# Performance work log

Measured on AMD Instinct MI355X. Metric: run time of the kernel, lower is better.

Reference implementation:

```python
import jax, jax.numpy as jnp
import numpy as np

D_MODEL = 1024
N_STATE = 64
BASEWIDTH = 3
BC_SCALE = (D_MODEL / BASEWIDTH) ** -0.5  # 'mup' mode width_mult**-0.5
RMS_EPS = 1.1920928955078125e-07  # torch.finfo(float32).eps (RMSNorm eps=None default)


def setup_inputs() -> dict:
    key = jax.random.key(0)
    k1, k2, k3, k4 = jax.random.split(key, 4)
    Bsz, L = 4, 2048
    u = jax.random.normal(k1, (Bsz, D_MODEL, L), dtype=jnp.float32)
    A = jax.random.uniform(k2, (N_STATE,), dtype=jnp.float32) * 0.1  # buffer: rand(N)*A_scale
    B = (jax.random.normal(k3, (N_STATE, D_MODEL), dtype=jnp.float32) + 0.1) * BC_SCALE
    C = (jax.random.normal(k4, (N_STATE, D_MODEL), dtype=jnp.float32) + 0.1) * BC_SCALE
    D = jnp.ones((D_MODEL,), dtype=jnp.float32)
    norm_w = jnp.ones((D_MODEL,), dtype=jnp.float32)
    return {"L": L, "u": u, "A": A, "B": B, "C": C, "D": D, "norm_w": norm_w}


def _ssm(u, A, B, C, D, norm_w):
    # u: [b, d, l]
    scale = BC_SCALE  # applied to Bu, Cu in 'mup' hyperparam mode
    Bu = jnp.einsum('nd,bdl->bnl', B, u) * scale  # [b, n, l]
    Cu = jnp.einsum('nd,bdl->bnl', C, u) * scale  # [b, n, l]
    b, d, l = u.shape
    # shifted_delta == 1 (delta path commented out in source), so
    # h_{t} = A * h_{t-1} + Bu[:, :, t] (outer) u[:, :, t]
    h0 = jnp.zeros((b, d, A.shape[0]), dtype=u.dtype)

    def step(h, xs):
        bu_t, cu_t, u_t = xs  # [b,n], [b,n], [b,d]
        h = h * A + u_t[:, :, None] * bu_t[:, None, :]  # [b, d, n]
        y_t = jnp.einsum('bn,bdn->bd', cu_t, h)
        return h, y_t

    xs = (jnp.moveaxis(Bu, 2, 0), jnp.moveaxis(Cu, 2, 0), jnp.moveaxis(u, 2, 0))
    _, y = jax.lax.scan(step, h0, xs)  # y: [l, b, d]
    y = jnp.moveaxis(y, 0, 2).transpose(1, 0, 2) if False else jnp.transpose(y, (1, 2, 0))  # [b, d, l]
    out = y + u * D[None, :, None]
    # RMSNorm over d_model (apply in [b, l, d] layout)
    x = jnp.transpose(out, (0, 2, 1))  # [b, l, d]
    ms = jnp.mean(x * x, axis=-1, keepdims=True)
    x = x * jax.lax.rsqrt(ms + RMS_EPS) * norm_w
    return jnp.transpose(x, (0, 2, 1))  # [b, d, l]


def reference(L, u, A, B, C, D, norm_w):
    del L  # sequence length == u.shape[-1]
    return _ssm(u, A, B, C, D, norm_w)
```

## Files before the change

kernel.cpp:

```cpp
#include <hip/hip_runtime.h>
#include <stdint.h>

#define DM 1024
#define LS 2048
#define RMS_EPS 1.1920928955078125e-07f
#define S2 0.0029296875f

typedef __attribute__((ext_vector_type(8))) short bf16x8;
typedef __attribute__((ext_vector_type(4))) float f32x4;

__device__ __forceinline__ unsigned short f2bf(float f) {
  uint32_t u = __builtin_bit_cast(uint32_t, f);
  u += 0x7FFFu + ((u >> 16) & 1u);
  return (unsigned short)(u >> 16);
}

__global__ __launch_bounds__(256) void k0_prep(const float* __restrict__ B,
                                               const float* __restrict__ C,
                                               unsigned short* __restrict__ Bbf) {
  int i4 = blockIdx.x * 256 + threadIdx.x;
  const float4* src = (i4 < 16384) ? (const float4*)B : (const float4*)C;
  float4 v = src[i4 & 16383];
  ushort4 o;
  o.x = f2bf(v.x); o.y = f2bf(v.y); o.z = f2bf(v.z); o.w = f2bf(v.w);
  ((ushort4*)Bbf)[i4] = o;
}

__global__ __launch_bounds__(256) void kg(const float* __restrict__ u,
                                          const unsigned short* __restrict__ Bbf,
                                          const float* __restrict__ A,
                                          float* __restrict__ Kwg) {
  const int wg = blockIdx.x;
  const int sw = (wg & 7) * 64 + (wg >> 3);
  const int b  = sw >> 7;
  const int t0 = (sw & 127) * 16;
  const int tid  = threadIdx.x;
  const int lane = tid & 63;
  const int w    = tid >> 6;
  const int nn = lane & 15, q = lane >> 4;
  const float* ub = u + (size_t)b * DM * LS;

  __shared__ __align__(16) bf16x8 tile[128][32];
  __shared__ float KwS[16][20];
  float (*BuCu)[132] = (float (*)[132])&tile[0][0];

  {
    const int kq = lane >> 3;
    const int lo = lane & 7;
    const int gcol = t0 - 16 + 4*lo;
    #pragma unroll
    for (int hh = 0; hh < 4; ++hh) {
      const int krow = 256*w + 32*kq + 8*hh;
      float4 vv[8];
      if (gcol >= 0) {
        #pragma unroll
        for (int r = 0; r < 8; ++r)
          vv[r] = *(const float4*)(ub + (size_t)(krow + r) * LS + gcol);
      } else {
        #pragma unroll
        for (int r = 0; r < 8; ++r) vv[r] = make_float4(0.f, 0.f, 0.f, 0.f);
      }
      const int k8 = krow >> 3;
      #pragma unroll
      for (int c = 0; c < 4; ++c) {
        union { bf16x8 v; unsigned short s[8]; } t8;
        #pragma unroll
        for (int r = 0; r < 8; ++r) t8.s[r] = f2bf(((const float*)&vv[r])[c]);
        tile[k8][(4*lo + c) ^ kq] = t8.v;
      }
    }
  }
  __syncthreads();

  f32x4 acc[2][2] = {};
  const unsigned short* arow0 = Bbf + (size_t)(32*w + nn) * DM + 8*q;
  #pragma unroll 4
  for (int it = 0; it < 32; ++it) {
    const int sx = nn ^ (it & 7);
    bf16x8 bf1 = tile[4*it + q][16 + sx];
    bf16x8 af0 = *(const bf16x8*)(arow0 + 32*it);
    bf16x8 af1 = *(const bf16x8*)(arow0 + (size_t)16*DM + 32*it);
    acc[0][1] = __builtin_amdgcn_mfma_f32_16x16x32_bf16(af0, bf1, acc[0][1], 0, 0, 0);
    acc[1][1] = __builtin_amdgcn_mfma_f32_16x16x32_bf16(af1, bf1, acc[1][1], 0, 0, 0);
    if (w < 2) {
      bf16x8 bf0 = tile[4*it + q][sx];
      acc[0][0] = __builtin_amdgcn_mfma_f32_16x16x32_bf16(af0, bf0, acc[0][0], 0, 0, 0);
      acc[1][0] = __builtin_amdgcn_mfma_f32_16x16x32_bf16(af1, bf0, acc[1][0], 0, 0, 0);
    }
  }
  __syncthreads();

  #pragma unroll
  for (int rt = 0; rt < 2; ++rt)
    #pragma unroll
    for (int cn = 0; cn < 2; ++cn)
      *(f32x4*)&BuCu[16*cn + nn][32*w + 16*rt + 4*q] = acc[rt][cn];
  __syncthreads();

  {
    const int t = tid >> 4, p = tid & 15;
    const float4 cu = *(const float4*)&BuCu[16 + t][64 + 4*p];
    const float4 aa = *(const float4*)(A + 4*p);
    float pw0 = cu.x * S2, pw1 = cu.y * S2, pw2 = cu.z * S2, pw3 = cu.w * S2;
    #pragma unroll
    for (int j = 0; j < 16; ++j) {
      const float4 b4 = *(const float4*)&BuCu[16 + t - j][4*p];
      float s = pw0*b4.x + pw1*b4.y + pw2*b4.z + pw3*b4.w;
      s += __shfl_xor(s, 1, 64);
      s += __shfl_xor(s, 2, 64);
      s += __shfl_xor(s, 4, 64);
      s += __shfl_xor(s, 8, 64);
      if (p == 0) KwS[t][j] = s;
      pw0 *= aa.x; pw1 *= aa.y; pw2 *= aa.z; pw3 *= aa.w;
    }
  }
  __syncthreads();
  if (tid < 64) {
    const int t = tid >> 2, jq = tid & 3;
    *(float4*)(Kwg + ((size_t)b * LS + t0 + t) * 16 + 4*jq) =
        *(const float4*)&KwS[t][4*jq];
  }
}

__global__ __launch_bounds__(512) void kc(const float* __restrict__ u,
                                          const float* __restrict__ Kwg,
                                          const float* __restrict__ Dv,
                                          const float* __restrict__ nw,
                                          float* __restrict__ out) {
  const int wg = blockIdx.x;
  const int sw = (wg & 7) * 64 + (wg >> 3);
  const int b  = sw >> 7;
  const int t0 = (sw & 127) * 16;
  const int tid  = threadIdx.x;
  const int lane = tid & 63;
  const int w    = tid >> 6;
  const float* ub = u + (size_t)b * DM * LS;
  float* ob = out + (size_t)b * DM * LS;

  __shared__ float KwS[16][20];
  __shared__ float SSr[8][16];
  __shared__ float rsqv[16];

  if (tid < 64) {
    const int t = tid >> 2, jq = tid & 3;
    *(float4*)&KwS[t][4*jq] =
        *(const float4*)(Kwg + ((size_t)b * LS + t0 + t) * 16 + 4*jq);
  }
  __syncthreads();

  const int tg = tid & 3;
  const int dr = tid >> 2;
  const int cbase = t0 - 16 + 4*tg;
  float y[8][4];
  float ps[4] = {0.f, 0.f, 0.f, 0.f};
  #pragma unroll 1
  for (int c = 0; c < 8; ++c) {
    const int d = dr + 128*c;
    const float* rowp = ub + (size_t)d * LS;
    float wr[20];
    #pragma unroll
    for (int s5 = 0; s5 < 5; ++s5) {
      int g = cbase + 4*s5;
      float4 v = (g >= 0) ? *(const float4*)(rowp + g)
                          : make_float4(0.f, 0.f, 0.f, 0.f);
      wr[4*s5+0] = v.x; wr[4*s5+1] = v.y; wr[4*s5+2] = v.z; wr[4*s5+3] = v.w;
    }
    const float Dd = Dv[d];
    #pragma unroll
    for (int k = 0; k < 4; ++k) {
      f32x4 kv0 = *(const f32x4*)&KwS[4*tg + k][0];
      f32x4 kv1 = *(const f32x4*)&KwS[4*tg + k][4];
      f32x4 kv2 = *(const f32x4*)&KwS[4*tg + k][8];
      f32x4 kv3 = *(const f32x4*)&KwS[4*tg + k][12];
      float acc = wr[16 + k] * Dd;
      #pragma unroll
      for (int j = 0; j < 4; ++j)  acc = fmaf(kv0[j], wr[16 + k - j],      acc);
      #pragma unroll
      for (int j = 0; j < 4; ++j)  acc = fmaf(kv1[j], wr[16 + k - (j+4)],  acc);
      #pragma unroll
      for (int j = 0; j < 4; ++j)  acc = fmaf(kv2[j], wr[16 + k - (j+8)],  acc);
      #pragma unroll
      for (int j = 0; j < 4; ++j)  acc = fmaf(kv3[j], wr[16 + k - (j+12)], acc);
      y[c][k] = acc;
      ps[k] = fmaf(acc, acc, ps[k]);
    }
  }

  #pragma unroll
  for (int k = 0; k < 4; ++k) {
    ps[k] += __shfl_xor(ps[k], 4, 64);
    ps[k] += __shfl_xor(ps[k], 8, 64);
    ps[k] += __shfl_xor(ps[k], 16, 64);
    ps[k] += __shfl_xor(ps[k], 32, 64);
  }
  if (lane < 4)
    *(float4*)&SSr[w][4*lane] = make_float4(ps[0], ps[1], ps[2], ps[3]);
  __syncthreads();
  if (tid < 16) {
    float s = 0.f;
    #pragma unroll
    for (int ww = 0; ww < 8; ++ww) s += SSr[ww][tid];
    rsqv[tid] = rsqrtf(s * (1.f/1024.f) + RMS_EPS);
  }
  __syncthreads();

  float rq[4];
  #pragma unroll
  for (int k = 0; k < 4; ++k) rq[k] = rsqv[4*tg + k];
  #pragma unroll 1
  for (int c = 0; c < 8; ++c) {
    const int d = dr + 128*c;
    const float wn2 = nw[d];
    float4 o;
    o.x = y[c][0] * rq[0] * wn2;
    o.y = y[c][1] * rq[1] * wn2;
    o.z = y[c][2] * rq[2] * wn2;
    o.w = y[c][3] * rq[3] * wn2;
    *(float4*)(ob + (size_t)d * LS + t0 + 4*tg) = o;
  }
}

extern "C" void kernel_launch(void* const* d_in, const int* in_sizes, int n_in,
                              void* d_out, int out_size, void* d_ws, size_t ws_size,
                              hipStream_t stream) {
  const float* u  = (const float*)d_in[1];
  const float* A  = (const float*)d_in[2];
  const float* B  = (const float*)d_in[3];
  const float* C  = (const float*)d_in[4];
  const float* Dv = (const float*)d_in[5];
  const float* nw = (const float*)d_in[6];
  float* out = (float*)d_out;

  float* Kwg = (float*)d_ws;
  unsigned short* Bbf = (unsigned short*)((char*)d_ws + (512u << 10));

  k0_prep<<<dim3(128), dim3(256), 0, stream>>>(B, C, Bbf);
  kg     <<<dim3(512), dim3(256), 0, stream>>>(u, Bbf, A, Kwg);
  kc     <<<dim3(512), dim3(512), 0, stream>>>(u, Kwg, Dv, nw, out);
}
```

Baseline: 145.1 us.

## Fuse kernel-weight generation and causal convolution with RMSNorm into one kernel

Merges the kg and kc kernels so that each workgroup reuses the bf16 u tile already staged in LDS for the 16-tap causal convolution, D skip and RMSNorm. This removes the second full read of u from global memory, the Kwg workspace round trip and one kernel launch. Bu/Cu are now stored as bf16 in LDS, and the convolution reads bf16 u instead of fp32, which lowers precision of the output path. Work is remapped so each thread covers 4 channels by 16 timesteps, which raises register pressure.

```diff
diff --git a/kernel.cpp b/kernel.cpp
--- a/kernel.cpp
+++ b/kernel.cpp
@@ -13,6 +13,10 @@
   uint32_t u = __builtin_bit_cast(uint32_t, f);
   u += 0x7FFFu + ((u >> 16) & 1u);
   return (unsigned short)(u >> 16);
+}
+__device__ __forceinline__ float bf2f(unsigned short s) {
+  uint32_t u = ((uint32_t)s) << 16;
+  return __builtin_bit_cast(float, u);
 }
 
 __global__ __launch_bounds__(256) void k0_prep(const float* __restrict__ B,
@@ -26,10 +30,12 @@
   ((ushort4*)Bbf)[i4] = o;
 }
 
-__global__ __launch_bounds__(256) void kg(const float* __restrict__ u,
+__global__ __launch_bounds__(256) void kf(const float* __restrict__ u,
                                           const unsigned short* __restrict__ Bbf,
                                           const float* __restrict__ A,
-                                          float* __restrict__ Kwg) {
+                                          const float* __restrict__ Dv,
+                                          const float* __restrict__ nw,
+                                          float* __restrict__ out) {
   const int wg = blockIdx.x;
   const int sw = (wg & 7) * 64 + (wg >> 3);
   const int b  = sw >> 7;
@@ -41,8 +47,13 @@
   const float* ub = u + (size_t)b * DM * LS;
 
   __shared__ __align__(16) bf16x8 tile[128][32];
-  __shared__ float KwS[16][20];
-  float (*BuCu)[132] = (float (*)[132])&tile[0][0];
+  __shared__ __align__(16) unsigned short BuCuB[32][136];
+  __shared__ __align__(16) float Kwd[32][16];
+  __shared__ float SSr[4][16];
+  __shared__ float rsqv[16];
+
+  ((float*)Kwd)[tid]       = 0.f;
+  ((float*)Kwd)[tid + 256] = 0.f;
 
   {
     const int kq = lane >> 3;
@@ -74,7 +85,7 @@
 
   f32x4 acc[2][2] = {};
   const unsigned short* arow0 = Bbf + (size_t)(32*w + nn) * DM + 8*q;
-  #pragma unroll 4
+  #pragma unroll 8
   for (int it = 0; it < 32; ++it) {
     const int sx = nn ^ (it & 7);
     bf16x8 bf1 = tile[4*it + q][16 + sx];
@@ -88,135 +99,128 @@
       acc[1][0] = __builtin_amdgcn_mfma_f32_16x16x32_bf16(af1, bf0, acc[1][0], 0, 0, 0);
     }
   }
-  __syncthreads();
 
   #pragma unroll
   for (int rt = 0; rt < 2; ++rt)
     #pragma unroll
-    for (int cn = 0; cn < 2; ++cn)
-      *(f32x4*)&BuCu[16*cn + nn][32*w + 16*rt + 4*q] = acc[rt][cn];
+    for (int cn = 0; cn < 2; ++cn) {
+      ushort4 pk;
+      pk.x = f2bf(acc[rt][cn][0]); pk.y = f2bf(acc[rt][cn][1]);
+      pk.z = f2bf(acc[rt][cn][2]); pk.w = f2bf(acc[rt][cn][3]);
+      *(ushort4*)&BuCuB[16*cn + nn][32*w + 16*rt + 4*q] = pk;
+    }
   __syncthreads();
 
   {
     const int t = tid >> 4, p = tid & 15;
-    const float4 cu = *(const float4*)&BuCu[16 + t][64 + 4*p];
+    const ushort4 cub = *(const ushort4*)&BuCuB[16 + t][64 + 4*p];
     const float4 aa = *(const float4*)(A + 4*p);
-    float pw0 = cu.x * S2, pw1 = cu.y * S2, pw2 = cu.z * S2, pw3 = cu.w * S2;
+    float pw0 = bf2f(cub.x) * S2, pw1 = bf2f(cub.y) * S2;
+    float pw2 = bf2f(cub.z) * S2, pw3 = bf2f(cub.w) * S2;
     #pragma unroll
     for (int j = 0; j < 16; ++j) {
-      const float4 b4 = *(const float4*)&BuCu[16 + t - j][4*p];
-      float s = pw0*b4.x + pw1*b4.y + pw2*b4.z + pw3*b4.w;
+      const ushort4 b4 = *(const ushort4*)&BuCuB[16 + t - j][4*p];
+      float s = pw0*bf2f(b4.x) + pw1*bf2f(b4.y) + pw2*bf2f(b4.z) + pw3*bf2f(b4.w);
       s += __shfl_xor(s, 1, 64);
       s += __shfl_xor(s, 2, 64);
       s += __shfl_xor(s, 4, 64);
       s += __shfl_xor(s, 8, 64);
-      if (p == 0) KwS[t][j] = s;
+      if (p == 0) Kwd[t + 16 - j][t] = s;
       pw0 *= aa.x; pw1 *= aa.y; pw2 *= aa.z; pw3 *= aa.w;
     }
   }
   __syncthreads();
-  if (tid < 64) {
-    const int t = tid >> 2, jq = tid & 3;
-    *(float4*)(Kwg + ((size_t)b * LS + t0 + t) * 16 + 4*jq) =
-        *(const float4*)&KwS[t][4*jq];
-  }
-}
-
-__global__ __launch_bounds__(512) void kc(const float* __restrict__ u,
-                                          const float* __restrict__ Kwg,
-                                          const float* __restrict__ Dv,
-                                          const float* __restrict__ nw,
-                                          float* __restrict__ out) {
-  const int wg = blockIdx.x;
-  const int sw = (wg & 7) * 64 + (wg >> 3);
-  const int b  = sw >> 7;
-  const int t0 = (sw & 127) * 16;
-  const int tid  = threadIdx.x;
-  const int lane = tid & 63;
-  const int w    = tid >> 6;
-  const float* ub = u + (size_t)b * DM * LS;
+
+  const int k8c = tid >> 1, hf = tid & 1;
+  const int kqc = (k8c >> 2) & 7;
+  const int d0 = 4 * tid;
+  float Dd[4];
+  #pragma unroll
+  for (int i = 0; i < 4; ++i) Dd[i] = Dv[d0 + i];
+  float y[4][16];
+  #pragma unroll
+  for (int d = 0; d < 4; ++d)
+    #pragma unroll
+    for (int t = 0; t < 16; ++t) y[d][t] = 0.f;
+
+  #pragma unroll
+  for (int s = 1; s < 32; ++s) {
+    const ushort4 uv = *(const ushort4*)((const char*)&tile[k8c][s ^ kqc] + 8*hf);
+    const float f0 = bf2f(uv.x), f1 = bf2f(uv.y), f2 = bf2f(uv.z), f3 = bf2f(uv.w);
+    const f32x4 kv0 = *(const f32x4*)&Kwd[s][0];
+    const f32x4 kv1 = *(const f32x4*)&Kwd[s][4];
+    const f32x4 kv2 = *(const f32x4*)&Kwd[s][8];
+    const f32x4 kv3 = *(const f32x4*)&Kwd[s][12];
+    const int tlo = (s >= 17) ? (s - 16) : 0;
+    const int thi = (s <= 16) ? (s - 1) : 15;
+    #pragma unroll
+    for (int t = 0; t < 16; ++t) {
+      if (t < tlo || t > thi) continue;
+      const float kvt = (t < 4) ? kv0[t] : (t < 8) ? kv1[t-4]
+                       : (t < 12) ? kv2[t-8] : kv3[t-12];
+      y[0][t] = fmaf(kvt, f0, y[0][t]);
+      y[1][t] = fmaf(kvt, f1, y[1][t]);
+      y[2][t] = fmaf(kvt, f2, y[2][t]);
+      y[3][t] = fmaf(kvt, f3, y[3][t]);
+    }
+    if (s >= 16) {
+      const int t = s - 16;
+      y[0][t] = fmaf(Dd[0], f0, y[0][t]);
+      y[1][t] = fmaf(Dd[1], f1, y[1][t]);
+      y[2][t] = fmaf(Dd[2], f2, y[2][t]);
+      y[3][t] = fmaf(Dd[3], f3, y[3][t]);
+    }
+  }
+
+  float ps[16];
+  #pragma unroll
+  for (int t = 0; t < 16; ++t)
+    ps[t] = fmaf(y[0][t], y[0][t], fmaf(y[1][t], y[1][t],
+            fmaf(y[2][t], y[2][t], y[3][t]*y[3][t])));
+  #pragma unroll
+  for (int t = 0; t < 16; ++t) {
+    ps[t] += __shfl_xor(ps[t], 1, 64);
+    ps[t] += __shfl_xor(ps[t], 2, 64);
+    ps[t] += __shfl_xor(ps[t], 4, 64);
+    ps[t] += __shfl_xor(ps[t], 8, 64);
+    ps[t] += __shfl_xor(ps[t], 16, 64);
+    ps[t] += __shfl_xor(ps[t], 32, 64);
+  }
+  if (lane == 0) {
+    *(float4*)&SSr[w][0]  = make_float4(ps[0],  ps[1],  ps[2],  ps[3]);
+    *(float4*)&SSr[w][4]  = make_float4(ps[4],  ps[5],  ps[6],  ps[7]);
+    *(float4*)&SSr[w][8]  = make_float4(ps[8],  ps[9],  ps[10], ps[11]);
+    *(float4*)&SSr[w][12] = make_float4(ps[12], ps[13], ps[14], ps[15]);
+  }
+  __syncthreads();
+  if (tid < 16) {
+    float s = SSr[0][tid] + SSr[1][tid] + SSr[2][tid] + SSr[3][tid];
+    rsqv[tid] = rsqrtf(s * (1.f/1024.f) + RMS_EPS);
+  }
+  __syncthreads();
+
+  const f32x4 rq0 = *(const f32x4*)&rsqv[0];
+  const f32x4 rq1 = *(const f32x4*)&rsqv[4];
+  const f32x4 rq2 = *(const f32x4*)&rsqv[8];
+  const f32x4 rq3 = *(const f32x4*)&rsqv[12];
   float* ob = out + (size_t)b * DM * LS;
-
-  __shared__ float KwS[16][20];
-  __shared__ float SSr[8][16];
-  __shared__ float rsqv[16];
-
-  if (tid < 64) {
-    const int t = tid >> 2, jq = tid & 3;
-    *(float4*)&KwS[t][4*jq] =
-        *(const float4*)(Kwg + ((size_t)b * LS + t0 + t) * 16 + 4*jq);
-  }
-  __syncthreads();
-
-  const int tg = tid & 3;
-  const int dr = tid >> 2;
-  const int cbase = t0 - 16 + 4*tg;
-  float y[8][4];
-  float ps[4] = {0.f, 0.f, 0.f, 0.f};
-  #pragma unroll 1
-  for (int c = 0; c < 8; ++c) {
-    const int d = dr + 128*c;
-    const float* rowp = ub + (size_t)d * LS;
-    float wr[20];
-    #pragma unroll
-    for (int s5 = 0; s5 < 5; ++s5) {
-      int g = cbase + 4*s5;
-      float4 v = (g >= 0) ? *(const float4*)(rowp + g)
-                          : make_float4(0.f, 0.f, 0.f, 0.f);
-      wr[4*s5+0] = v.x; wr[4*s5+1] = v.y; wr[4*s5+2] = v.z; wr[4*s5+3] = v.w;
-    }
-    const float Dd = Dv[d];
-    #pragma unroll
-    for (int k = 0; k < 4; ++k) {
-      f32x4 kv0 = *(const f32x4*)&KwS[4*tg + k][0];
-      f32x4 kv1 = *(const f32x4*)&KwS[4*tg + k][4];
-      f32x4 kv2 = *(const f32x4*)&KwS[4*tg + k][8];
-      f32x4 kv3 = *(const f32x4*)&KwS[4*tg + k][12];
-      float acc = wr[16 + k] * Dd;
-      #pragma unroll
-      for (int j = 0; j < 4; ++j)  acc = fmaf(kv0[j], wr[16 + k - j],      acc);
-      #pragma unroll
-      for (int j = 0; j < 4; ++j)  acc = fmaf(kv1[j], wr[16 + k - (j+4)],  acc);
-      #pragma unroll
-      for (int j = 0; j < 4; ++j)  acc = fmaf(kv2[j], wr[16 + k - (j+8)],  acc);
-      #pragma unroll
-      for (int j = 0; j < 4; ++j)  acc = fmaf(kv3[j], wr[16 + k - (j+12)], acc);
-      y[c][k] = acc;
-      ps[k] = fmaf(acc, acc, ps[k]);
-    }
-  }
-
-  #pragma unroll
-  for (int k = 0; k < 4; ++k) {
-    ps[k] += __shfl_xor(ps[k], 4, 64);
-    ps[k] += __shfl_xor(ps[k], 8, 64);
-    ps[k] += __shfl_xor(ps[k], 16, 64);
-    ps[k] += __shfl_xor(ps[k], 32, 64);
-  }
-  if (lane < 4)
-    *(float4*)&SSr[w][4*lane] = make_float4(ps[0], ps[1], ps[2], ps[3]);
-  __syncthreads();
-  if (tid < 16) {
-    float s = 0.f;
-    #pragma unroll
-    for (int ww = 0; ww < 8; ++ww) s += SSr[ww][tid];
-    rsqv[tid] = rsqrtf(s * (1.f/1024.f) + RMS_EPS);
-  }
-  __syncthreads();
-
-  float rq[4];
-  #pragma unroll
-  for (int k = 0; k < 4; ++k) rq[k] = rsqv[4*tg + k];
-  #pragma unroll 1
-  for (int c = 0; c < 8; ++c) {
-    const int d = dr + 128*c;
-    const float wn2 = nw[d];
+  #pragma unroll
+  for (int d = 0; d < 4; ++d) {
+    const float wn2 = nw[d0 + d];
+    float* orow = ob + (size_t)(d0 + d) * LS + t0;
     float4 o;
-    o.x = y[c][0] * rq[0] * wn2;
-    o.y = y[c][1] * rq[1] * wn2;
-    o.z = y[c][2] * rq[2] * wn2;
-    o.w = y[c][3] * rq[3] * wn2;
-    *(float4*)(ob + (size_t)d * LS + t0 + 4*tg) = o;
+    o.x = y[d][0]*rq0[0]*wn2;  o.y = y[d][1]*rq0[1]*wn2;
+    o.z = y[d][2]*rq0[2]*wn2;  o.w = y[d][3]*rq0[3]*wn2;
+    *(float4*)(orow + 0) = o;
+    o.x = y[d][4]*rq1[0]*wn2;  o.y = y[d][5]*rq1[1]*wn2;
+    o.z = y[d][6]*rq1[2]*wn2;  o.w = y[d][7]*rq1[3]*wn2;
+    *(float4*)(orow + 4) = o;
+    o.x = y[d][8]*rq2[0]*wn2;  o.y = y[d][9]*rq2[1]*wn2;
+    o.z = y[d][10]*rq2[2]*wn2; o.w = y[d][11]*rq2[3]*wn2;
+    *(float4*)(orow + 8) = o;
+    o.x = y[d][12]*rq3[0]*wn2; o.y = y[d][13]*rq3[1]*wn2;
+    o.z = y[d][14]*rq3[2]*wn2; o.w = y[d][15]*rq3[3]*wn2;
+    *(float4*)(orow + 12) = o;
   }
 }
 
@@ -231,10 +235,8 @@
   const float* nw = (const float*)d_in[6];
   float* out = (float*)d_out;
 
-  float* Kwg = (float*)d_ws;
-  unsigned short* Bbf = (unsigned short*)((char*)d_ws + (512u << 10));
+  unsigned short* Bbf = (unsigned short*)d_ws;
 
   k0_prep<<<dim3(128), dim3(256), 0, stream>>>(B, C, Bbf);
-  kg     <<<dim3(512), dim3(256), 0, stream>>>(u, Bbf, A, Kwg);
-  kc     <<<dim3(512), dim3(512), 0, stream>>>(u, Kwg, Dv, nw, out);
-}
+  kf     <<<dim3(512), dim3(256), 0, stream>>>(u, Bbf, A, Dv, nw, out);
+}
```

Result: no change. 146.0 us (+0.6%).

## Split GEMM and kernel-weight computation into separate kernels to drop halo recompute

Applied to the files above, without the earlier changes.

The fused kg kernel, which recomputed Bu/Cu for a 16-step halo in each workgroup, is split in two. k1_gemm computes Bu/Cu for exactly 16 timesteps per block and writes them transposed to a global workspace. A new kwx kernel then reads neighboring timesteps from global memory to build the 16-tap weights. This halves the MFMA work and the u reads in the GEMM stage, at the cost of an extra kernel launch and a global round trip through a roughly 4 MB intermediate buffer.

```diff
diff --git a/kernel.cpp b/kernel.cpp
--- a/kernel.cpp
+++ b/kernel.cpp
@@ -26,85 +26,82 @@
   ((ushort4*)Bbf)[i4] = o;
 }
 
-__global__ __launch_bounds__(256) void kg(const float* __restrict__ u,
-                                          const unsigned short* __restrict__ Bbf,
-                                          const float* __restrict__ A,
-                                          float* __restrict__ Kwg) {
-  const int wg = blockIdx.x;
-  const int sw = (wg & 7) * 64 + (wg >> 3);
-  const int b  = sw >> 7;
-  const int t0 = (sw & 127) * 16;
-  const int tid  = threadIdx.x;
-  const int lane = tid & 63;
-  const int w    = tid >> 6;
-  const int nn = lane & 15, q = lane >> 4;
+__global__ __launch_bounds__(256) void k1_gemm(const float* __restrict__ u,
+                                               const unsigned short* __restrict__ Bbf,
+                                               float* __restrict__ BuCuT) {
+  const int b    = blockIdx.y;
+  const int l0   = blockIdx.x * 16;
+  const int lane = threadIdx.x & 63;
+  const int w    = threadIdx.x >> 6;
   const float* ub = u + (size_t)b * DM * LS;
 
-  __shared__ __align__(16) bf16x8 tile[128][32];
-  __shared__ float KwS[16][20];
-  float (*BuCu)[132] = (float (*)[132])&tile[0][0];
+  __shared__ bf16x8 tile[128][16];
 
   {
-    const int kq = lane >> 3;
-    const int lo = lane & 7;
-    const int gcol = t0 - 16 + 4*lo;
-    #pragma unroll
-    for (int hh = 0; hh < 4; ++hh) {
-      const int krow = 256*w + 32*kq + 8*hh;
+    const int lq = lane & 3;
+    const int kg = lane >> 2;
+    const int kbase = 256 * w + 16 * kg;
+    #pragma unroll
+    for (int h = 0; h < 2; ++h) {
       float4 vv[8];
-      if (gcol >= 0) {
+      #pragma unroll
+      for (int r = 0; r < 8; ++r)
+        vv[r] = *(const float4*)(ub + (size_t)(kbase + 8*h + r) * LS + l0 + 4*lq);
+      const int k8 = 32*w + 2*kg + h;
+      #pragma unroll
+      for (int c = 0; c < 4; ++c) {
+        union { bf16x8 v; unsigned short s[8]; } t;
         #pragma unroll
-        for (int r = 0; r < 8; ++r)
-          vv[r] = *(const float4*)(ub + (size_t)(krow + r) * LS + gcol);
-      } else {
-        #pragma unroll
-        for (int r = 0; r < 8; ++r) vv[r] = make_float4(0.f, 0.f, 0.f, 0.f);
+        for (int r = 0; r < 8; ++r) t.s[r] = f2bf(((const float*)&vv[r])[c]);
+        tile[k8][(4*lq + c) ^ (k8 & 3)] = t.v;
       }
-      const int k8 = krow >> 3;
-      #pragma unroll
-      for (int c = 0; c < 4; ++c) {
-        union { bf16x8 v; unsigned short s[8]; } t8;
-        #pragma unroll
-        for (int r = 0; r < 8; ++r) t8.s[r] = f2bf(((const float*)&vv[r])[c]);
-        tile[k8][(4*lo + c) ^ kq] = t8.v;
-      }
-    }
-  }
-  __syncthreads();
-
-  f32x4 acc[2][2] = {};
-  const unsigned short* arow0 = Bbf + (size_t)(32*w + nn) * DM + 8*q;
+    }
+  }
+  __syncthreads();
+
+  const int n = lane & 15;
+  const int q = lane >> 4;
+  f32x4 acc[2] = {};
   #pragma unroll 4
   for (int it = 0; it < 32; ++it) {
-    const int sx = nn ^ (it & 7);
-    bf16x8 bf1 = tile[4*it + q][16 + sx];
-    bf16x8 af0 = *(const bf16x8*)(arow0 + 32*it);
-    bf16x8 af1 = *(const bf16x8*)(arow0 + (size_t)16*DM + 32*it);
-    acc[0][1] = __builtin_amdgcn_mfma_f32_16x16x32_bf16(af0, bf1, acc[0][1], 0, 0, 0);
-    acc[1][1] = __builtin_amdgcn_mfma_f32_16x16x32_bf16(af1, bf1, acc[1][1], 0, 0, 0);
-    if (w < 2) {
-      bf16x8 bf0 = tile[4*it + q][sx];
-      acc[0][0] = __builtin_amdgcn_mfma_f32_16x16x32_bf16(af0, bf0, acc[0][0], 0, 0, 0);
-      acc[1][0] = __builtin_amdgcn_mfma_f32_16x16x32_bf16(af1, bf0, acc[1][0], 0, 0, 0);
-    }
-  }
-  __syncthreads();
-
+    bf16x8 bfrag = tile[4*it + q][n ^ q];
+    #pragma unroll
+    for (int rt = 0; rt < 2; ++rt) {
+      int row = 32*w + 16*rt + n;
+      bf16x8 a = *(const bf16x8*)(Bbf + (size_t)row * DM + 32*it + 8*q);
+      acc[rt] = __builtin_amdgcn_mfma_f32_16x16x32_bf16(a, bfrag, acc[rt], 0, 0, 0);
+    }
+  }
+
+  float* ob = BuCuT + (size_t)b * LS * 128;
   #pragma unroll
-  for (int rt = 0; rt < 2; ++rt)
-    #pragma unroll
-    for (int cn = 0; cn < 2; ++cn)
-      *(f32x4*)&BuCu[16*cn + nn][32*w + 16*rt + 4*q] = acc[rt][cn];
-  __syncthreads();
+  for (int rt = 0; rt < 2; ++rt) {
+    int col = l0 + n;
+    int row = 32*w + 16*rt + 4*q;
+    *(f32x4*)(ob + (size_t)col * 128 + row) = acc[rt];
+  }
+}
+
+__global__ __launch_bounds__(256) void kwx(const float* __restrict__ BuCuT,
+                                           const float* __restrict__ A,
+                                           float* __restrict__ Kwg) {
+  const int b  = blockIdx.y;
+  const int t0 = blockIdx.x * 16;
+  const int tid = threadIdx.x;
+
+  __shared__ float KwS[16][20];
 
   {
     const int t = tid >> 4, p = tid & 15;
-    const float4 cu = *(const float4*)&BuCu[16 + t][64 + 4*p];
+    const float* bb = BuCuT + (size_t)b * LS * 128;
+    const float4 cu = *(const float4*)(bb + (size_t)(t0 + t) * 128 + 64 + 4*p);
     const float4 aa = *(const float4*)(A + 4*p);
     float pw0 = cu.x * S2, pw1 = cu.y * S2, pw2 = cu.z * S2, pw3 = cu.w * S2;
     #pragma unroll
     for (int j = 0; j < 16; ++j) {
-      const float4 b4 = *(const float4*)&BuCu[16 + t - j][4*p];
+      const int g = t0 + t - j;
+      const float4 b4 = (g >= 0) ? *(const float4*)(bb + (size_t)g * 128 + 4*p)
+                                 : make_float4(0.f, 0.f, 0.f, 0.f);
       float s = pw0*b4.x + pw1*b4.y + pw2*b4.z + pw3*b4.w;
       s += __shfl_xor(s, 1, 64);
       s += __shfl_xor(s, 2, 64);
@@ -231,10 +228,12 @@
   const float* nw = (const float*)d_in[6];
   float* out = (float*)d_out;
 
-  float* Kwg = (float*)d_ws;
-  unsigned short* Bbf = (unsigned short*)((char*)d_ws + (512u << 10));
-
-  k0_prep<<<dim3(128), dim3(256), 0, stream>>>(B, C, Bbf);
-  kg     <<<dim3(512), dim3(256), 0, stream>>>(u, Bbf, A, Kwg);
-  kc     <<<dim3(512), dim3(512), 0, stream>>>(u, Kwg, Dv, nw, out);
-}
+  float* BuCuT = (float*)d_ws;
+  unsigned short* Bbf = (unsigned short*)((char*)d_ws + (4u << 20));
+  float* Kwg = (float*)((char*)d_ws + (4u << 20) + (256u << 10));
+
+  k0_prep<<<dim3(128),    dim3(256), 0, stream>>>(B, C, Bbf);
+  k1_gemm<<<dim3(128, 4), dim3(256), 0, stream>>>(u, Bbf, BuCuT);
+  kwx    <<<dim3(128, 4), dim3(256), 0, stream>>>(BuCuT, A, Kwg);
+  kc     <<<dim3(512),    dim3(512), 0, stream>>>(u, Kwg, Dv, nw, out);
+}
```

New measurement: 155.2 us. +6.9%, slower.
